# Kernel tuning notes

Hardware: AMD Instinct MI355X
Metric: run time of the kernel (lower is better)

## Reference

```python
import jax, jax.numpy as jnp
import numpy as np

B, W, H = 16384, 16, 16
NUM_CLASSES = 1024
EMBED = 4
OUT = 1024

def setup_inputs() -> dict:
    key = jax.random.key(0)
    k0, k1, k2 = jax.random.split(key, 3)
    x = jax.random.randint(k0, (B, W, H), 0, NUM_CLASSES, dtype=jnp.int32)
    W_embed = jax.random.normal(k1, (NUM_CLASSES, EMBED), dtype=jnp.float32) * 0.02
    b_embed = jnp.zeros((EMBED,), dtype=jnp.float32)
    W_dense = jax.random.normal(k2, (EMBED * W * H, OUT), dtype=jnp.float32) * 0.02
    b_dense = jnp.zeros((OUT,), dtype=jnp.float32)
    return {"x": x, "W_embed": W_embed, "b_embed": b_embed, "W_dense": W_dense, "b_dense": b_dense}

def reference(x, W_embed, b_embed, W_dense, b_dense):
    # one_hot(x, C) @ W_embed + b_embed is mathematically a row-gather of W_embed
    emb = W_embed[x] + b_embed                 # (B, W, H, EMBED)
    flat = emb.reshape(emb.shape[0], -1)        # (B, W*H*EMBED)  == rearrange '... w h c -> ... (w h c)'
    return flat @ W_dense + b_dense             # (B, OUT)
```

## Files before the change

kernel.cpp:

```cpp
#include <hip/hip_runtime.h>
#include <stdint.h>
#include <stddef.h>

typedef __attribute__((ext_vector_type(8))) short bf16x8;
typedef __attribute__((ext_vector_type(8))) unsigned short u16x8;
typedef __attribute__((ext_vector_type(4))) float f32x4;

typedef const __attribute__((address_space(1))) void* gptr1_t;
typedef __attribute__((address_space(3))) void* lptr3_t;

#define GLOAD_LDS16(gp, lp) \
  __builtin_amdgcn_global_load_lds((gptr1_t)(gp), (lptr3_t)(lp), 16, 0, 0)

__device__ __forceinline__ uint16_t f2bf(float f) {
  uint32_t u = __builtin_bit_cast(uint32_t, f);
  u += 0x7fffu + ((u >> 16) & 1u);
  return (uint16_t)(u >> 16);
}

#define MB   16384
#define NP   256
#define KDIM 1024
#define NDIM 1024

__global__ void build_a_kernel(const int* __restrict__ x,
                               const float* __restrict__ We,
                               const float* __restrict__ be,
                               uint16_t* __restrict__ A) {
  const int t = blockIdx.x * 256 + threadIdx.x;
  const int2 cls = ((const int2*)x)[t];
  const float4 e0 = *(const float4*)(We + (size_t)cls.x * 4);
  const float4 e1 = *(const float4*)(We + (size_t)cls.y * 4);
  const float4 bb = *(const float4*)be;
  u16x8 o = { f2bf(e0.x + bb.x), f2bf(e0.y + bb.y), f2bf(e0.z + bb.z), f2bf(e0.w + bb.w),
              f2bf(e1.x + bb.x), f2bf(e1.y + bb.y), f2bf(e1.z + bb.z), f2bf(e1.w + bb.w) };
  *(u16x8*)(A + (size_t)t * 8) = o;
}

__global__ void build_bt_kernel(const float* __restrict__ Wd,
                                uint16_t* __restrict__ Bt) {
  __shared__ uint16_t tile[32][33];
  const int k0 = blockIdx.y * 32;
  const int n0 = blockIdx.x * 32;
  const int tx = threadIdx.x;
  const int ty = threadIdx.y;
  #pragma unroll
  for (int r = 0; r < 32; r += 8)
    tile[ty + r][tx] = f2bf(Wd[(size_t)(k0 + ty + r) * NDIM + n0 + tx]);
  __syncthreads();
  #pragma unroll
  for (int r = 0; r < 32; r += 8)
    Bt[(size_t)(n0 + ty + r) * KDIM + k0 + tx] = tile[tx][ty + r];
}

#define BM  128
#define BN  128
#define BKH 32
#define BK  64
#define NK  (KDIM / BK)

__global__ __launch_bounds__(256) void gemm_bt_kernel(
    const uint16_t* __restrict__ A,
    const uint16_t* __restrict__ Bt,
    const float* __restrict__ bias,
    float* __restrict__ C) {
  __shared__ uint16_t As[2][BM * BKH];
  __shared__ uint16_t Bs[2][BN * BKH];

  const int tid  = threadIdx.x;
  const int bm   = blockIdx.x;
  const int bn   = blockIdx.y;
  const int wave = tid >> 6;
  const int lane = tid & 63;
  const int wr   = wave >> 1;
  const int wc   = wave & 1;
  const int lm   = lane & 15;
  const int q    = lane >> 4;

  const int row0 = bm * BM;
  const int col0 = bn * BN;

  const int srow = tid >> 2;
  const int scol = (tid & 3) * 8;

  f32x4 acc[4][4];
  #pragma unroll
  for (int i = 0; i < 4; i++)
    #pragma unroll
    for (int j = 0; j < 4; j++)
      acc[i][j] = (f32x4){0.f, 0.f, 0.f, 0.f};

  for (int kt = 0; kt < NK; ++kt) {
    const int k0 = kt * BK;
    #pragma unroll
    for (int h = 0; h < 2; ++h) {
      GLOAD_LDS16(A  + (size_t)(row0      + srow) * KDIM + k0 + h * BKH + scol, As[h] + tid * 8);
      GLOAD_LDS16(A  + (size_t)(row0 + 64 + srow) * KDIM + k0 + h * BKH + scol, As[h] + 2048 + tid * 8);
      GLOAD_LDS16(Bt + (size_t)(col0      + srow) * KDIM + k0 + h * BKH + scol, Bs[h] + tid * 8);
      GLOAD_LDS16(Bt + (size_t)(col0 + 64 + srow) * KDIM + k0 + h * BKH + scol, Bs[h] + 2048 + tid * 8);
    }
    __syncthreads();

    #pragma unroll
    for (int h = 0; h < 2; ++h) {
      bf16x8 af[4], bfr[4];
      #pragma unroll
      for (int i = 0; i < 4; i++)
        af[i] = *(const bf16x8*)(As[h] + (wr * 64 + i * 16 + lm) * BKH + q * 8);
      #pragma unroll
      for (int j = 0; j < 4; j++)
        bfr[j] = *(const bf16x8*)(Bs[h] + (wc * 64 + j * 16 + lm) * BKH + q * 8);

      #pragma unroll
      for (int i = 0; i < 4; i++)
        #pragma unroll
        for (int j = 0; j < 4; j++)
          acc[i][j] = __builtin_amdgcn_mfma_f32_16x16x32_bf16(af[i], bfr[j], acc[i][j], 0, 0, 0);
    }

    __syncthreads();
  }

  float bvals[4];
  #pragma unroll
  for (int j = 0; j < 4; j++)
    bvals[j] = bias[col0 + wc * 64 + j * 16 + lm];

  #pragma unroll
  for (int i = 0; i < 4; i++) {
    const int rbase = row0 + wr * 64 + i * 16 + q * 4;
    #pragma unroll
    for (int j = 0; j < 4; j++) {
      const int col = col0 + wc * 64 + j * 16 + lm;
      #pragma unroll
      for (int r = 0; r < 4; r++)
        C[(size_t)(rbase + r) * NDIM + col] = acc[i][j][r] + bvals[j];
    }
  }
}

__global__ void naive_kernel(const int* __restrict__ x,
                             const float* __restrict__ We,
                             const float* __restrict__ be,
                             const float* __restrict__ Wd,
                             const float* __restrict__ bd,
                             float* __restrict__ out) {
  __shared__ float emb[KDIM];
  const int b = blockIdx.x;
  const int tid = threadIdx.x;
  {
    const int cls = x[(size_t)b * NP + tid];
    const float4 e  = *(const float4*)(We + (size_t)cls * 4);
    const float4 bb = *(const float4*)be;
    emb[tid * 4 + 0] = e.x + bb.x;
    emb[tid * 4 + 1] = e.y + bb.y;
    emb[tid * 4 + 2] = e.z + bb.z;
    emb[tid * 4 + 3] = e.w + bb.w;
  }
  __syncthreads();
  float acc0 = bd[tid], acc1 = bd[tid + 256], acc2 = bd[tid + 512], acc3 = bd[tid + 768];
  for (int k = 0; k < KDIM; ++k) {
    const float a = emb[k];
    const float* w = Wd + (size_t)k * NDIM + tid;
    acc0 += a * w[0];
    acc1 += a * w[256];
    acc2 += a * w[512];
    acc3 += a * w[768];
  }
  float* o = out + (size_t)b * NDIM + tid;
  o[0] = acc0; o[256] = acc1; o[512] = acc2; o[768] = acc3;
}

extern "C" void kernel_launch(void* const* d_in, const int* in_sizes, int n_in,
                              void* d_out, int out_size, void* d_ws, size_t ws_size,
                              hipStream_t stream) {
  const int*   x  = (const int*)d_in[0];
  const float* We = (const float*)d_in[1];
  const float* be = (const float*)d_in[2];
  const float* Wd = (const float*)d_in[3];
  const float* bd = (const float*)d_in[4];
  float* out = (float*)d_out;

  const size_t needA = (size_t)MB * KDIM * sizeof(uint16_t);
  const size_t needB = (size_t)NDIM * KDIM * sizeof(uint16_t);

  if (ws_size >= needA + needB) {
    uint16_t* Aw  = (uint16_t*)d_ws;
    uint16_t* Btw = (uint16_t*)((char*)d_ws + needA);
    build_a_kernel<<<MB * NP / 2 / 256, 256, 0, stream>>>(x, We, be, Aw);
    build_bt_kernel<<<dim3(NDIM / 32, KDIM / 32), dim3(32, 8), 0, stream>>>(Wd, Btw);
    gemm_bt_kernel<<<dim3(MB / BM, NDIM / BN), 256, 0, stream>>>(Aw, Btw, bd, out);
  } else {
    naive_kernel<<<MB, 256, 0, stream>>>(x, We, be, Wd, bd, out);
  }
}
```

Measured before the change: 133.8 us.

## Fuse embedding gather into GEMM A-tile load via LDS lookup table

Drops the separate kernel that materialized the 32MB bf16 embedding matrix A. Each GEMM block now copies a small bf16 embedding table into LDS, reads the class indices directly, and gathers rows from that table to fill the A tiles in shared memory, prefetching the next indices one step ahead. The bf16 table conversion is folded into the Bt transpose kernel. This removes a large write and re-read of A through global memory, at the cost of extra LDS use (8KB) and LDS gather traffic and stores inside the main loop, where they contend with the MFMA work.

```diff
diff --git a/kernel.cpp b/kernel.cpp
--- a/kernel.cpp
+++ b/kernel.cpp
@@ -23,22 +23,11 @@
 #define KDIM 1024
 #define NDIM 1024
 
-__global__ void build_a_kernel(const int* __restrict__ x,
-                               const float* __restrict__ We,
-                               const float* __restrict__ be,
-                               uint16_t* __restrict__ A) {
-  const int t = blockIdx.x * 256 + threadIdx.x;
-  const int2 cls = ((const int2*)x)[t];
-  const float4 e0 = *(const float4*)(We + (size_t)cls.x * 4);
-  const float4 e1 = *(const float4*)(We + (size_t)cls.y * 4);
-  const float4 bb = *(const float4*)be;
-  u16x8 o = { f2bf(e0.x + bb.x), f2bf(e0.y + bb.y), f2bf(e0.z + bb.z), f2bf(e0.w + bb.w),
-              f2bf(e1.x + bb.x), f2bf(e1.y + bb.y), f2bf(e1.z + bb.z), f2bf(e1.w + bb.w) };
-  *(u16x8*)(A + (size_t)t * 8) = o;
-}
-
-__global__ void build_bt_kernel(const float* __restrict__ Wd,
-                                uint16_t* __restrict__ Bt) {
+__global__ void build_bt_webf_kernel(const float* __restrict__ Wd,
+                                     const float* __restrict__ We,
+                                     const float* __restrict__ be,
+                                     uint16_t* __restrict__ Bt,
+                                     uint16_t* __restrict__ Webf) {
   __shared__ uint16_t tile[32][33];
   const int k0 = blockIdx.y * 32;
   const int n0 = blockIdx.x * 32;
@@ -51,6 +40,19 @@
   #pragma unroll
   for (int r = 0; r < 32; r += 8)
     Bt[(size_t)(n0 + ty + r) * KDIM + k0 + tx] = tile[tx][ty + r];
+
+  if (blockIdx.x == 0 && blockIdx.y == 0) {
+    const int flat = ty * 32 + tx;
+    const float4 bb = *(const float4*)be;
+    #pragma unroll
+    for (int c = 0; c < 4; ++c) {
+      const int cls = flat * 4 + c;
+      const float4 e = *(const float4*)(We + (size_t)cls * 4);
+      ushort4 o = { f2bf(e.x + bb.x), f2bf(e.y + bb.y),
+                    f2bf(e.z + bb.z), f2bf(e.w + bb.w) };
+      *(ushort4*)(Webf + (size_t)cls * 4) = o;
+    }
+  }
 }
 
 #define BM  128
@@ -59,13 +61,15 @@
 #define BK  64
 #define NK  (KDIM / BK)
 
-__global__ __launch_bounds__(256) void gemm_bt_kernel(
-    const uint16_t* __restrict__ A,
+__global__ __launch_bounds__(256) void gemm_fused_kernel(
+    const int* __restrict__ x,
+    const uint16_t* __restrict__ Webf,
     const uint16_t* __restrict__ Bt,
     const float* __restrict__ bias,
     float* __restrict__ C) {
   __shared__ uint16_t As[2][BM * BKH];
   __shared__ uint16_t Bs[2][BN * BKH];
+  __shared__ uint16_t Tab[KDIM * 4];
 
   const int tid  = threadIdx.x;
   const int bm   = blockIdx.x;
@@ -83,6 +87,36 @@
   const int srow = tid >> 2;
   const int scol = (tid & 3) * 8;
 
+  const int pc = (tid & 3) * 2;
+  const int* xr0 = x + (size_t)(row0 + srow)      * NP + pc;
+  const int* xr1 = x + (size_t)(row0 + 64 + srow) * NP + pc;
+
+  int2 xa0 = *(const int2*)(xr0);
+  int2 xb0 = *(const int2*)(xr0 + 8);
+  int2 xa1 = *(const int2*)(xr1);
+  int2 xb1 = *(const int2*)(xr1 + 8);
+
+  {
+    u16x8 t0 = *(const u16x8*)(Webf + tid * 16);
+    u16x8 t1 = *(const u16x8*)(Webf + tid * 16 + 8);
+    *(u16x8*)(Tab + tid * 16)     = t0;
+    *(u16x8*)(Tab + tid * 16 + 8) = t1;
+  }
+  __syncthreads();
+
+  ushort4 g[8];
+#define GATHER_ALL()                                          \
+  g[0] = *(const ushort4*)(Tab + (size_t)xa0.x * 4);          \
+  g[1] = *(const ushort4*)(Tab + (size_t)xa0.y * 4);          \
+  g[2] = *(const ushort4*)(Tab + (size_t)xb0.x * 4);          \
+  g[3] = *(const ushort4*)(Tab + (size_t)xb0.y * 4);          \
+  g[4] = *(const ushort4*)(Tab + (size_t)xa1.x * 4);          \
+  g[5] = *(const ushort4*)(Tab + (size_t)xa1.y * 4);          \
+  g[6] = *(const ushort4*)(Tab + (size_t)xb1.x * 4);          \
+  g[7] = *(const ushort4*)(Tab + (size_t)xb1.y * 4);
+
+  GATHER_ALL();
+
   f32x4 acc[4][4];
   #pragma unroll
   for (int i = 0; i < 4; i++)
@@ -92,14 +126,29 @@
 
   for (int kt = 0; kt < NK; ++kt) {
     const int k0 = kt * BK;
+
     #pragma unroll
     for (int h = 0; h < 2; ++h) {
-      GLOAD_LDS16(A  + (size_t)(row0      + srow) * KDIM + k0 + h * BKH + scol, As[h] + tid * 8);
-      GLOAD_LDS16(A  + (size_t)(row0 + 64 + srow) * KDIM + k0 + h * BKH + scol, As[h] + 2048 + tid * 8);
       GLOAD_LDS16(Bt + (size_t)(col0      + srow) * KDIM + k0 + h * BKH + scol, Bs[h] + tid * 8);
       GLOAD_LDS16(Bt + (size_t)(col0 + 64 + srow) * KDIM + k0 + h * BKH + scol, Bs[h] + 2048 + tid * 8);
     }
+
+    if (kt + 1 < NK) {
+      const int off = (kt + 1) * 16;
+      xa0 = *(const int2*)(xr0 + off);
+      xb0 = *(const int2*)(xr0 + off + 8);
+      xa1 = *(const int2*)(xr1 + off);
+      xb1 = *(const int2*)(xr1 + off + 8);
+    }
+
+    *(u16x8*)(As[0] + tid * 8)        = (u16x8){ g[0].x,g[0].y,g[0].z,g[0].w, g[1].x,g[1].y,g[1].z,g[1].w };
+    *(u16x8*)(As[1] + tid * 8)        = (u16x8){ g[2].x,g[2].y,g[2].z,g[2].w, g[3].x,g[3].y,g[3].z,g[3].w };
+    *(u16x8*)(As[0] + 2048 + tid * 8) = (u16x8){ g[4].x,g[4].y,g[4].z,g[4].w, g[5].x,g[5].y,g[5].z,g[5].w };
+    *(u16x8*)(As[1] + 2048 + tid * 8) = (u16x8){ g[6].x,g[6].y,g[6].z,g[6].w, g[7].x,g[7].y,g[7].z,g[7].w };
+
     __syncthreads();
+
+    GATHER_ALL();
 
     #pragma unroll
     for (int h = 0; h < 2; ++h) {
@@ -181,15 +230,14 @@
   const float* bd = (const float*)d_in[4];
   float* out = (float*)d_out;
 
-  const size_t needA = (size_t)MB * KDIM * sizeof(uint16_t);
+  const size_t needW = (size_t)KDIM * 4 * sizeof(uint16_t);
   const size_t needB = (size_t)NDIM * KDIM * sizeof(uint16_t);
 
-  if (ws_size >= needA + needB) {
-    uint16_t* Aw  = (uint16_t*)d_ws;
-    uint16_t* Btw = (uint16_t*)((char*)d_ws + needA);
-    build_a_kernel<<<MB * NP / 2 / 256, 256, 0, stream>>>(x, We, be, Aw);
-    build_bt_kernel<<<dim3(NDIM / 32, KDIM / 32), dim3(32, 8), 0, stream>>>(Wd, Btw);
-    gemm_bt_kernel<<<dim3(MB / BM, NDIM / BN), 256, 0, stream>>>(Aw, Btw, bd, out);
+  if (ws_size >= needW + needB) {
+    uint16_t* Webf = (uint16_t*)d_ws;
+    uint16_t* Btw  = (uint16_t*)((char*)d_ws + needW);
+    build_bt_webf_kernel<<<dim3(NDIM / 32, KDIM / 32), dim3(32, 8), 0, stream>>>(Wd, We, be, Btw, Webf);
+    gemm_fused_kernel<<<dim3(MB / BM, NDIM / BN), 256, 0, stream>>>(x, Webf, Btw, bd, out);
   } else {
     naive_kernel<<<MB, 256, 0, stream>>>(x, We, be, Wd, bd, out);
   }
```

After: 149.9 us. 12.0% more time.
